# Optimization experiments

Hardware: AMD Instinct MI355X
Metric: run time of the kernel (lower is better)

Reference implementation:

```python
import jax, jax.numpy as jnp
import numpy as np
from jax import lax

N_STATES = 512
VOCAB = 32000
BATCH = 16
SEQ_LEN = 128


def setup_inputs() -> dict:
    key = jax.random.key(0)
    k_ids, k_em, k_tm, k_p = jax.random.split(key, 4)
    input_ids = jax.random.randint(k_ids, (BATCH, SEQ_LEN), 0, VOCAB, dtype=jnp.int64)
    em = jax.random.normal(k_em, (N_STATES, VOCAB), dtype=jnp.float32)
    tm = jax.random.normal(k_tm, (N_STATES, N_STATES), dtype=jnp.float32)
    p = jax.random.normal(k_p, (N_STATES,), dtype=jnp.float32)
    return {"input_ids": input_ids, "em": em, "tm": tm, "p": p}


def reference(input_ids, em, tm, p):
    """HMM forward algorithm in log space; returns mean NLL (scalar).

    em: [S, V] emission logits, tm: [S, S] transition logits, p: [S] prior logits.
    do_log_softmax=True -> normalize each in log space first.
    """
    log_em = jax.nn.log_softmax(em, axis=-1)   # [S, V]
    log_tm = jax.nn.log_softmax(tm, axis=-1)   # [S, S] rows = source state
    log_p = jax.nn.log_softmax(p, axis=-1)     # [S]

    # Gather emission log-probs per token: [B, T, S]
    em_tok = log_em.T[input_ids]

    # alpha_0[b, s] = log_p[s] + log_em[s, x_0]
    alpha0 = log_p[None, :] + em_tok[:, 0]     # [B, S]

    def step(alpha, e_t):
        # alpha: [B, S_src]; log-matmul: logsumexp over source states
        a = jax.nn.logsumexp(alpha[:, :, None] + log_tm[None, :, :], axis=1) + e_t
        return a, None

    em_rest = jnp.swapaxes(em_tok[:, 1:], 0, 1)  # [T-1, B, S]
    alpha_T, _ = lax.scan(step, alpha0, em_rest)

    # loss = -mean_b log p(x_b) = -mean_b logsumexp_s alpha_T[b, s]
    loss = -jnp.mean(jax.nn.logsumexp(alpha_T, axis=-1))
    return loss
```

## Files before the change

### kernel.cpp

```cpp
#include <hip/hip_runtime.h>
#include <hip/hip_bf16.h>

#define NS 512
#define NV 32000
#define NB 16
#define NT 128

#ifndef __has_builtin
#define __has_builtin(x) 0
#endif

typedef int v8i __attribute__((ext_vector_type(8)));
typedef float v4f __attribute__((ext_vector_type(4)));

__device__ inline unsigned enc_e4m3(float x) {
    x = fminf(x, 448.0f);
    unsigned u = __float_as_uint(x);
    if (x < 0.015625f) {
        return (unsigned)(int)rintf(x * 512.0f);
    }
    unsigned u2 = u + 0x7FFFFu + ((u >> 20) & 1u);
    return (((u2 >> 23) - 120u) << 3) | ((u2 >> 20) & 7u);
}

__device__ inline unsigned pack4_e4m3(float a, float b, float c, float d) {
#if __has_builtin(__builtin_amdgcn_cvt_pk_fp8_f32)
    int v = __builtin_amdgcn_cvt_pk_fp8_f32(a, b, 0, false);
    v = __builtin_amdgcn_cvt_pk_fp8_f32(c, d, v, true);
    return (unsigned)v;
#else
    return enc_e4m3(a) | (enc_e4m3(b) << 8) | (enc_e4m3(c) << 16) | (enc_e4m3(d) << 24);
#endif
}

#define DPPMAX(x, ctrl) \
    x = fmaxf(x, __int_as_float(__builtin_amdgcn_mov_dpp(__float_as_int(x), ctrl, 0xF, 0xF, true)))
#define DPPADD(x, ctrl) \
    x = x + __int_as_float(__builtin_amdgcn_mov_dpp(__float_as_int(x), ctrl, 0xF, 0xF, true))

#define UMX(a, b) ((a) > (b) ? (a) : (b))

__device__ inline unsigned bytemax8(unsigned a, unsigned b) {
    unsigned m0 = UMX(a & 255u, b & 255u);
    unsigned m1 = UMX((a >> 8) & 255u, (b >> 8) & 255u);
    unsigned m2 = UMX((a >> 16) & 255u, (b >> 16) & 255u);
    unsigned m3 = UMX(a >> 24, b >> 24);
    return UMX(UMX(m0, m1), UMX(m2, m3));
}

__global__ __launch_bounds__(256) void k_emtok_T(
    const float* __restrict__ em, const int* __restrict__ ids,
    float* __restrict__ em_lin_T)
{
    const int s   = blockIdx.x;
    const int tid = threadIdx.x;
    const float* row = em + (size_t)s * NV;

    int idv[8];
#pragma unroll
    for (int k = 0; k < 8; ++k) idv[k] = ids[tid + 256 * k];
    float g[8];
#pragma unroll
    for (int k = 0; k < 8; ++k) g[k] = row[idv[k]];

    float sum = 0.f;
    const float4* row4 = (const float4*)row;
#pragma unroll 4
    for (int i = 0; i < 31; ++i) {
        float4 v = row4[tid + 256 * i];
        sum += __expf(v.x) + __expf(v.y) + __expf(v.z) + __expf(v.w);
    }
    sum += __expf(row[31744 + tid]);

#pragma unroll
    for (int off = 32; off; off >>= 1) sum += __shfl_down(sum, off);
    __shared__ float red[4];
    __shared__ float s_scale;
    if ((tid & 63) == 0) red[tid >> 6] = sum;
    __syncthreads();
    if (tid == 0) s_scale = (1.0f / ((red[0] + red[1]) + (red[2] + red[3]))) * 0x1p-18f;
    __syncthreads();
    const float scale = s_scale;

#pragma unroll
    for (int k = 0; k < 8; ++k)
        em_lin_T[(size_t)s * (NB * NT) + tid + 256 * k] = __expf(g[k]) * scale;
}

__global__ __launch_bounds__(256) void k_tr(
    const float* __restrict__ emT, float* __restrict__ em_lin)
{
    __shared__ float tile[32][33];
    const int jb = blockIdx.x * 32;
    const int sb = blockIdx.y * 32;
    const int cc = threadIdx.x & 31;
    const int rr = threadIdx.x >> 5;
#pragma unroll
    for (int i = 0; i < 4; ++i) {
        int r = rr + 8 * i;
        tile[r][cc] = emT[(size_t)(sb + r) * (NB * NT) + jb + cc];
    }
    __syncthreads();
#pragma unroll
    for (int i = 0; i < 4; ++i) {
        int r = rr + 8 * i;
        int s = sb + cc;
        int ps = (s & ~63) | ((s & 15) << 2) | ((s >> 4) & 3);
        em_lin[(size_t)(jb + r) * NS + ps] = tile[cc][r];
    }
}

__global__ __launch_bounds__(64) void k_z(
    const float* __restrict__ tm, float* __restrict__ zscale)
{
    const int k    = blockIdx.x;
    const int lane = threadIdx.x;
    const float* row = tm + (size_t)k * NS;

    float4 a = ((const float4*)row)[lane * 2];
    float4 b = ((const float4*)row)[lane * 2 + 1];
    float sum = ((__expf(a.x) + __expf(a.y)) + (__expf(a.z) + __expf(a.w)))
              + ((__expf(b.x) + __expf(b.y)) + (__expf(b.z) + __expf(b.w)));
#pragma unroll
    for (int off = 32; off; off >>= 1) sum += __shfl_down(sum, off);
    if (lane == 0) zscale[k] = 1024.0f / sum;
}

__global__ __launch_bounds__(256) void k_pt2(
    const float* __restrict__ tm, const float* __restrict__ zscale,
    unsigned char* __restrict__ PT)
{
    __shared__ float tile[64][65];
    __shared__ float zs[64];
    const int kb  = blockIdx.x * 64;
    const int db  = blockIdx.y * 64;
    const int tid = threadIdx.x;
    const int c   = tid & 63;
    const int r0  = tid >> 6;

    if (tid < 64) zs[tid] = zscale[kb + tid];
#pragma unroll
    for (int i = 0; i < 16; ++i) {
        int r = r0 + 4 * i;
        tile[r][c] = tm[(size_t)(kb + r) * NS + db + c];
    }
    __syncthreads();

    const int d  = tid >> 2;
    const int ks = (tid & 3) * 16;
    unsigned px[4];
#pragma unroll
    for (int gq = 0; gq < 4; ++gq) {
        int k0 = ks + gq * 4;
        px[gq] = pack4_e4m3(__expf(tile[k0 + 0][d]) * zs[k0 + 0],
                            __expf(tile[k0 + 1][d]) * zs[k0 + 1],
                            __expf(tile[k0 + 2][d]) * zs[k0 + 2],
                            __expf(tile[k0 + 3][d]) * zs[k0 + 3]);
    }
    uint4 o; o.x = px[0]; o.y = px[1]; o.z = px[2]; o.w = px[3];
    *(uint4*)(PT + (size_t)(db + d) * NS + kb + ks) = o;
}

__global__ __launch_bounds__(512, 2) void k_scan(
    const float* __restrict__ em_lin, const unsigned char* __restrict__ PT,
    const float* __restrict__ p, float* __restrict__ out)
{
    const int bb  = blockIdx.x;
    const int tid = threadIdx.x;
    const int w   = tid >> 6;
    const int l   = tid & 63;
    const int lc  = l & 15;
    const int lq  = l >> 4;

    __shared__ unsigned Ew[2][16 * 128];
    __shared__ __align__(4) unsigned char wmE2[2][32];
    __shared__ __align__(4) unsigned char mbuf[2][4];
    __shared__ float    wm2[8][4];
    __shared__ float    sbuf[4];

    v8i B[4][4];
#pragma unroll
    for (int nt = 0; nt < 4; ++nt) {
#pragma unroll
        for (int kt = 0; kt < 4; ++kt) {
            const uint4* src = (const uint4*)(PT + (size_t)((w * 4 + nt) * 16 + lc) * NS + kt * 128 + lq * 32);
            v8i bb8;
            *(uint4*)&bb8       = src[0];
            *((uint4*)&bb8 + 1) = src[1];
            B[nt][kt] = bb8;
        }
    }

    float zp = 0.f;
#pragma unroll
    for (int i = 0; i < 8; ++i) zp += __expf(p[l * 8 + i]);
    DPPADD(zp, 0x128); DPPADD(zp, 0x124); DPPADD(zp, 0xB1); DPPADD(zp, 0x4E);
    float Zp = __int_as_float(__builtin_amdgcn_readlane(__float_as_int(zp), 0))
             + __int_as_float(__builtin_amdgcn_readlane(__float_as_int(zp), 16))
             + __int_as_float(__builtin_amdgcn_readlane(__float_as_int(zp), 32))
             + __int_as_float(__builtin_amdgcn_readlane(__float_as_int(zp), 48));
    const float invZp = 1.0f / Zp;

    const int dbase0 = w * 64 + lc;
    const int gb     = bb * 4 + lq;

    const float* epb0 = em_lin + (size_t)gb * (NT * NS) + (w * 64 + lc * 4);
    v4f e0 = *(const v4f*)epb0;
    float alpha[4];
#pragma unroll
    for (int nt = 0; nt < 4; ++nt)
        alpha[nt] = __expf(p[dbase0 + 16 * nt]) * invZp * e0[nt];

    int gsum = 18;
    const unsigned sel1 = (l & 1) ? 0x07030501u : 0x02060004u;
    const unsigned sel2 = (l & 2) ? 0x07060302u : 0x01000504u;
    const int mrow = 4 * lq + (l & 3);

    int aidx[8];
#pragma unroll
    for (int kt = 0; kt < 4; ++kt) {
#pragma unroll
        for (int c = 0; c < 2; ++c)
            aidx[kt * 2 + c] = lc * 32 + (((kt * 8 + lq * 2 + c) ^ lc) & 31);
    }
    int widx[4];
#pragma unroll
    for (int nt = 0; nt < 4; ++nt)
        widx[nt] = mrow * 128 + ((((w * 4 + nt) ^ mrow) & 31) << 2) + (lc >> 2);

    const int bA = lc >> 2;
    const int h  = lq >> 1;
    const int wexp_w = (w & 1) * 16 + lq * 4 + (w >> 1);
    const int wexp_r = h * 16 + bA * 4;
    const unsigned shA = (unsigned)(bA << 3);
    const unsigned shQ = (unsigned)(lq << 3);

    const float* epb = epb0 + NS;

    {
        float mx = fmaxf(fmaxf(alpha[0], alpha[1]), fmaxf(alpha[2], alpha[3]));
        DPPMAX(mx, 0x128); DPPMAX(mx, 0x124); DPPMAX(mx, 0xB1); DPPMAX(mx, 0x4E);
        unsigned E = __float_as_uint(mx) >> 23;
        E = E > 1u ? E : 1u;
        if (lc == 0) wmE2[1][wexp_w] = (unsigned char)E;
    }
    __syncthreads();
    if (tid < 4) {
        const unsigned u0 = *(const unsigned*)&wmE2[1][tid * 4];
        const unsigned u1 = *(const unsigned*)&wmE2[1][16 + tid * 4];
        mbuf[1][tid] = (unsigned char)bytemax8(u0, u1);
    }

    const v4f CZ = {0.f, 0.f, 0.f, 0.f};

    for (int t = 1; t < NT; ++t) {
        const int buf = t & 1;
        unsigned* EwB = &Ew[buf][0];

        v4f epf = *(const v4f*)epb;
        epb += NS;

        float mx = fmaxf(fmaxf(alpha[0], alpha[1]), fmaxf(alpha[2], alpha[3]));
        DPPMAX(mx, 0x128); DPPMAX(mx, 0x124); DPPMAX(mx, 0xB1); DPPMAX(mx, 0x4E);
        unsigned E = __float_as_uint(mx) >> 23;
        E = E > 1u ? E : 1u;
        const float sc = __uint_as_float((261u - E) << 23);

#pragma unroll
        for (int nt = 0; nt < 4; ++nt) {
            unsigned dw = pack4_e4m3(alpha[nt] * sc, 0.f, 0.f, 0.f);
            int tmp = __builtin_amdgcn_mov_dpp((int)dw, 0xB1, 0xF, 0xF, true);
            dw = __builtin_amdgcn_perm(dw, (unsigned)tmp, sel1);
            tmp = __builtin_amdgcn_mov_dpp((int)dw, 0x4E, 0xF, 0xF, true);
            dw = __builtin_amdgcn_perm(dw, (unsigned)tmp, sel2);
            EwB[widx[nt]] = dw;
        }
        if (lc == 0) wmE2[buf][wexp_w] = (unsigned char)E;
        __syncthreads();

        v8i A[4];
        const uint4* eb4 = (const uint4*)EwB;
#pragma unroll
        for (int kt = 0; kt < 4; ++kt) {
            v8i aa;
            *(uint4*)&aa       = eb4[aidx[kt * 2 + 0]];
            *((uint4*)&aa + 1) = eb4[aidx[kt * 2 + 1]];
            A[kt] = aa;
        }

        if (tid < 4) {
            const unsigned u0 = *(const unsigned*)&wmE2[buf][tid * 4];
            const unsigned u1 = *(const unsigned*)&wmE2[buf][16 + tid * 4];
            mbuf[buf ^ 1][tid] = (unsigned char)bytemax8(u0, u1);
        }

        const unsigned mdw = *(const unsigned*)&mbuf[buf][0];
        const int MhA = (int)((mdw >> shA) & 255u);
        const int MhQ = (int)((mdw >> shQ) & 255u);
        gsum += MhQ - 126;

        const unsigned dwE = *(const unsigned*)&wmE2[buf][wexp_r];
        const int base = 127 - MhA;
        int s0 = (int)(dwE & 255u) + base;         s0 = s0 < 0 ? 0 : (s0 > 254 ? 254 : s0);
        int s1 = (int)((dwE >> 8) & 255u) + base;  s1 = s1 < 0 ? 0 : (s1 > 254 ? 254 : s1);
        int s2 = (int)((dwE >> 16) & 255u) + base; s2 = s2 < 0 ? 0 : (s2 > 254 ? 254 : s2);
        int s3 = (int)(dwE >> 24) + base;          s3 = s3 < 0 ? 0 : (s3 > 254 ? 254 : s3);
        const int scA[4] = { s0 * 0x01010101, s1 * 0x01010101,
                             s2 * 0x01010101, s3 * 0x01010101 };

        v4f C[4];
#pragma unroll
        for (int nt = 0; nt < 4; ++nt)
            C[nt] = __builtin_amdgcn_mfma_scale_f32_16x16x128_f8f6f4(
                        A[0], B[nt][0], CZ, 0, 0, 0, scA[0], 0, 0x7F7F7F7F);
#pragma unroll
        for (int kt = 1; kt < 4; ++kt)
#pragma unroll
            for (int nt = 0; nt < 4; ++nt)
                C[nt] = __builtin_amdgcn_mfma_scale_f32_16x16x128_f8f6f4(
                            A[kt], B[nt][kt], C[nt], 0, 0, 0, scA[kt], 0, 0x7F7F7F7F);

#pragma unroll
        for (int nt = 0; nt < 4; ++nt)
            alpha[nt] = C[nt][0] * epf[nt];
    }

    {
        float sm = (alpha[0] + alpha[1]) + (alpha[2] + alpha[3]);
        DPPADD(sm, 0x128); DPPADD(sm, 0x124); DPPADD(sm, 0xB1); DPPADD(sm, 0x4E);
        if (lc == 0) wm2[w][lq] = sm;
        if (w == 0 && lc == 0) sbuf[lq] = (float)gsum;
    }
    __syncthreads();
    if (tid < 4) {
        float s8 = ((wm2[0][tid] + wm2[1][tid]) + (wm2[2][tid] + wm2[3][tid]))
                 + ((wm2[4][tid] + wm2[5][tid]) + (wm2[6][tid] + wm2[7][tid]));
        float L2 = __log2f(s8) + sbuf[tid];
        atomicAdd(out, -(0.693147180559945f / 16.0f) * L2);
    }
}

extern "C" void kernel_launch(void* const* d_in, const int* in_sizes, int n_in,
                              void* d_out, int out_size, void* d_ws, size_t ws_size,
                              hipStream_t stream)
{
    const int*   ids = (const int*)d_in[0];
    const float* em  = (const float*)d_in[1];
    const float* tm  = (const float*)d_in[2];
    const float* p   = (const float*)d_in[3];
    float* out = (float*)d_out;

    float*          em_lin = (float*)d_ws;
    unsigned char*  PT     = (unsigned char*)d_ws + ((size_t)4 << 20);
    float*          zscale = (float*)((unsigned char*)d_ws + ((size_t)4 << 20) + ((size_t)256 << 10));
    float*          emT    = (float*)((unsigned char*)d_ws + ((size_t)4 << 20) + ((size_t)512 << 10));

    hipMemsetAsync(d_out, 0, sizeof(float), stream);

    k_emtok_T<<<NS, 256, 0, stream>>>(em, ids, emT);
    k_tr<<<dim3(64, 16), 256, 0, stream>>>(emT, em_lin);
    k_z<<<NS, 64, 0, stream>>>(tm, zscale);
    k_pt2<<<dim3(8, 8), 256, 0, stream>>>(tm, zscale, PT);
    k_scan<<<4, 512, 0, stream>>>(em_lin, PT, p, out);
}
```

Measured before the change: 244.6 us.

## Split scan work across 16 waves per block instead of 8

The sequential HMM scan kernel moves from 512 to 1024 threads per block, so each wave owns 32 destination states (two MFMA N-tiles) instead of 64. This halves the per-step MFMA chain and the B-register footprint per wave, aiming to shorten the latency of each serial timestep. In exchange, the per-wave exponent bookkeeping is reorganised into a 64-byte shared table, and every barrier now has to synchronise twice as many waves.

```diff
diff --git a/kernel.cpp b/kernel.cpp
--- a/kernel.cpp
+++ b/kernel.cpp
@@ -12,6 +12,7 @@
 
 typedef int v8i __attribute__((ext_vector_type(8)));
 typedef float v4f __attribute__((ext_vector_type(4)));
+typedef float v2f __attribute__((ext_vector_type(2)));
 
 __device__ inline unsigned enc_e4m3(float x) {
     x = fminf(x, 448.0f);
@@ -161,7 +162,7 @@
     *(uint4*)(PT + (size_t)(db + d) * NS + kb + ks) = o;
 }
 
-__global__ __launch_bounds__(512, 2) void k_scan(
+__global__ __launch_bounds__(1024, 1) void k_scan(
     const float* __restrict__ em_lin, const unsigned char* __restrict__ PT,
     const float* __restrict__ p, float* __restrict__ out)
 {
@@ -173,17 +174,17 @@
     const int lq  = l >> 4;
 
     __shared__ unsigned Ew[2][16 * 128];
-    __shared__ __align__(4) unsigned char wmE2[2][32];
+    __shared__ __align__(16) unsigned char wmE3[2][64];
     __shared__ __align__(4) unsigned char mbuf[2][4];
-    __shared__ float    wm2[8][4];
+    __shared__ float    wm2[16][4];
     __shared__ float    sbuf[4];
 
-    v8i B[4][4];
-#pragma unroll
-    for (int nt = 0; nt < 4; ++nt) {
+    v8i B[2][4];
+#pragma unroll
+    for (int nt = 0; nt < 2; ++nt) {
 #pragma unroll
         for (int kt = 0; kt < 4; ++kt) {
-            const uint4* src = (const uint4*)(PT + (size_t)((w * 4 + nt) * 16 + lc) * NS + kt * 128 + lq * 32);
+            const uint4* src = (const uint4*)(PT + (size_t)(w * 32 + nt * 16 + lc) * NS + kt * 128 + lq * 32);
             v8i bb8;
             *(uint4*)&bb8       = src[0];
             *((uint4*)&bb8 + 1) = src[1];
@@ -201,20 +202,21 @@
              + __int_as_float(__builtin_amdgcn_readlane(__float_as_int(zp), 48));
     const float invZp = 1.0f / Zp;
 
-    const int dbase0 = w * 64 + lc;
-    const int gb     = bb * 4 + lq;
-
-    const float* epb0 = em_lin + (size_t)gb * (NT * NS) + (w * 64 + lc * 4);
-    v4f e0 = *(const v4f*)epb0;
-    float alpha[4];
-#pragma unroll
-    for (int nt = 0; nt < 4; ++nt)
-        alpha[nt] = __expf(p[dbase0 + 16 * nt]) * invZp * e0[nt];
+    const int dbase = w * 32 + lc;
+    const int gb    = bb * 4 + lq;
+
+    const float* epb0 = em_lin + (size_t)gb * (NT * NS) + ((w >> 1) * 64 + lc * 4 + (w & 1) * 2);
+    v2f e0 = *(const v2f*)epb0;
+    float alpha[2];
+#pragma unroll
+    for (int nt = 0; nt < 2; ++nt)
+        alpha[nt] = __expf(p[dbase + 16 * nt]) * invZp * e0[nt];
 
     int gsum = 18;
     const unsigned sel1 = (l & 1) ? 0x07030501u : 0x02060004u;
     const unsigned sel2 = (l & 2) ? 0x07060302u : 0x01000504u;
     const int mrow = 4 * lq + (l & 3);
+    const int lcq  = (l >> 2) & 3;
 
     int aidx[8];
 #pragma unroll
@@ -223,32 +225,30 @@
         for (int c = 0; c < 2; ++c)
             aidx[kt * 2 + c] = lc * 32 + (((kt * 8 + lq * 2 + c) ^ lc) & 31);
     }
-    int widx[4];
-#pragma unroll
-    for (int nt = 0; nt < 4; ++nt)
-        widx[nt] = mrow * 128 + ((((w * 4 + nt) ^ mrow) & 31) << 2) + (lc >> 2);
+    int widx[2];
+#pragma unroll
+    for (int nt = 0; nt < 2; ++nt)
+        widx[nt] = mrow * 128 + ((((w * 2 + nt) ^ mrow) & 31) << 2) + lcq;
 
     const int bA = lc >> 2;
-    const int h  = lq >> 1;
-    const int wexp_w = (w & 1) * 16 + lq * 4 + (w >> 1);
-    const int wexp_r = h * 16 + bA * 4;
     const unsigned shA = (unsigned)(bA << 3);
     const unsigned shQ = (unsigned)(lq << 3);
+    const unsigned shK = (unsigned)(lq << 3);
+    const int wexp_w = (lq * 4 + (w >> 2)) * 4 + (w & 3);
 
     const float* epb = epb0 + NS;
 
     {
-        float mx = fmaxf(fmaxf(alpha[0], alpha[1]), fmaxf(alpha[2], alpha[3]));
+        float mx = fmaxf(alpha[0], alpha[1]);
         DPPMAX(mx, 0x128); DPPMAX(mx, 0x124); DPPMAX(mx, 0xB1); DPPMAX(mx, 0x4E);
         unsigned E = __float_as_uint(mx) >> 23;
         E = E > 1u ? E : 1u;
-        if (lc == 0) wmE2[1][wexp_w] = (unsigned char)E;
+        if (lc == 0) wmE3[1][wexp_w] = (unsigned char)E;
     }
     __syncthreads();
     if (tid < 4) {
-        const unsigned u0 = *(const unsigned*)&wmE2[1][tid * 4];
-        const unsigned u1 = *(const unsigned*)&wmE2[1][16 + tid * 4];
-        mbuf[1][tid] = (unsigned char)bytemax8(u0, u1);
+        const uint4 u = *(const uint4*)&wmE3[1][tid * 16];
+        mbuf[1][tid] = (unsigned char)bytemax8(bytemax8(u.x, u.y), bytemax8(u.z, u.w));
     }
 
     const v4f CZ = {0.f, 0.f, 0.f, 0.f};
@@ -257,17 +257,17 @@
         const int buf = t & 1;
         unsigned* EwB = &Ew[buf][0];
 
-        v4f epf = *(const v4f*)epb;
+        v2f epf = *(const v2f*)epb;
         epb += NS;
 
-        float mx = fmaxf(fmaxf(alpha[0], alpha[1]), fmaxf(alpha[2], alpha[3]));
+        float mx = fmaxf(alpha[0], alpha[1]);
         DPPMAX(mx, 0x128); DPPMAX(mx, 0x124); DPPMAX(mx, 0xB1); DPPMAX(mx, 0x4E);
         unsigned E = __float_as_uint(mx) >> 23;
         E = E > 1u ? E : 1u;
         const float sc = __uint_as_float((261u - E) << 23);
 
 #pragma unroll
-        for (int nt = 0; nt < 4; ++nt) {
+        for (int nt = 0; nt < 2; ++nt) {
             unsigned dw = pack4_e4m3(alpha[nt] * sc, 0.f, 0.f, 0.f);
             int tmp = __builtin_amdgcn_mov_dpp((int)dw, 0xB1, 0xF, 0xF, true);
             dw = __builtin_amdgcn_perm(dw, (unsigned)tmp, sel1);
@@ -275,7 +275,7 @@
             dw = __builtin_amdgcn_perm(dw, (unsigned)tmp, sel2);
             EwB[widx[nt]] = dw;
         }
-        if (lc == 0) wmE2[buf][wexp_w] = (unsigned char)E;
+        if (lc == 0) wmE3[buf][wexp_w] = (unsigned char)E;
         __syncthreads();
 
         v8i A[4];
@@ -289,9 +289,8 @@
         }
 
         if (tid < 4) {
-            const unsigned u0 = *(const unsigned*)&wmE2[buf][tid * 4];
-            const unsigned u1 = *(const unsigned*)&wmE2[buf][16 + tid * 4];
-            mbuf[buf ^ 1][tid] = (unsigned char)bytemax8(u0, u1);
+            const uint4 u = *(const uint4*)&wmE3[buf][tid * 16];
+            mbuf[buf ^ 1][tid] = (unsigned char)bytemax8(bytemax8(u.x, u.y), bytemax8(u.z, u.w));
         }
 
         const unsigned mdw = *(const unsigned*)&mbuf[buf][0];
@@ -299,42 +298,43 @@
         const int MhQ = (int)((mdw >> shQ) & 255u);
         gsum += MhQ - 126;
 
-        const unsigned dwE = *(const unsigned*)&wmE2[buf][wexp_r];
+        const uint4 ue = *(const uint4*)&wmE3[buf][bA * 16];
         const int base = 127 - MhA;
-        int s0 = (int)(dwE & 255u) + base;         s0 = s0 < 0 ? 0 : (s0 > 254 ? 254 : s0);
-        int s1 = (int)((dwE >> 8) & 255u) + base;  s1 = s1 < 0 ? 0 : (s1 > 254 ? 254 : s1);
-        int s2 = (int)((dwE >> 16) & 255u) + base; s2 = s2 < 0 ? 0 : (s2 > 254 ? 254 : s2);
-        int s3 = (int)(dwE >> 24) + base;          s3 = s3 < 0 ? 0 : (s3 > 254 ? 254 : s3);
+        int s0 = (int)((ue.x >> shK) & 255u) + base; s0 = s0 < 0 ? 0 : (s0 > 254 ? 254 : s0);
+        int s1 = (int)((ue.y >> shK) & 255u) + base; s1 = s1 < 0 ? 0 : (s1 > 254 ? 254 : s1);
+        int s2 = (int)((ue.z >> shK) & 255u) + base; s2 = s2 < 0 ? 0 : (s2 > 254 ? 254 : s2);
+        int s3 = (int)((ue.w >> shK) & 255u) + base; s3 = s3 < 0 ? 0 : (s3 > 254 ? 254 : s3);
         const int scA[4] = { s0 * 0x01010101, s1 * 0x01010101,
                              s2 * 0x01010101, s3 * 0x01010101 };
 
-        v4f C[4];
-#pragma unroll
-        for (int nt = 0; nt < 4; ++nt)
+        v4f C[2];
+#pragma unroll
+        for (int nt = 0; nt < 2; ++nt)
             C[nt] = __builtin_amdgcn_mfma_scale_f32_16x16x128_f8f6f4(
                         A[0], B[nt][0], CZ, 0, 0, 0, scA[0], 0, 0x7F7F7F7F);
 #pragma unroll
         for (int kt = 1; kt < 4; ++kt)
 #pragma unroll
-            for (int nt = 0; nt < 4; ++nt)
+            for (int nt = 0; nt < 2; ++nt)
                 C[nt] = __builtin_amdgcn_mfma_scale_f32_16x16x128_f8f6f4(
                             A[kt], B[nt][kt], C[nt], 0, 0, 0, scA[kt], 0, 0x7F7F7F7F);
 
 #pragma unroll
-        for (int nt = 0; nt < 4; ++nt)
+        for (int nt = 0; nt < 2; ++nt)
             alpha[nt] = C[nt][0] * epf[nt];
     }
 
     {
-        float sm = (alpha[0] + alpha[1]) + (alpha[2] + alpha[3]);
+        float sm = alpha[0] + alpha[1];
         DPPADD(sm, 0x128); DPPADD(sm, 0x124); DPPADD(sm, 0xB1); DPPADD(sm, 0x4E);
         if (lc == 0) wm2[w][lq] = sm;
         if (w == 0 && lc == 0) sbuf[lq] = (float)gsum;
     }
     __syncthreads();
     if (tid < 4) {
-        float s8 = ((wm2[0][tid] + wm2[1][tid]) + (wm2[2][tid] + wm2[3][tid]))
-                 + ((wm2[4][tid] + wm2[5][tid]) + (wm2[6][tid] + wm2[7][tid]));
+        float s8 = 0.f;
+#pragma unroll
+        for (int i = 0; i < 16; ++i) s8 += wm2[i][tid];
         float L2 = __log2f(s8) + sbuf[tid];
         atomicAdd(out, -(0.693147180559945f / 16.0f) * L2);
     }
@@ -361,5 +361,5 @@
     k_tr<<<dim3(64, 16), 256, 0, stream>>>(emT, em_lin);
     k_z<<<NS, 64, 0, stream>>>(tm, zscale);
     k_pt2<<<dim3(8, 8), 256, 0, stream>>>(tm, zscale, PT);
-    k_scan<<<4, 512, 0, stream>>>(em_lin, PT, p, out);
-}
+    k_scan<<<4, 1024, 0, stream>>>(em_lin, PT, p, out);
+}
```

Result: slower. 430.6 us (+76.0%).
